# Performance work log

Hardware: AMD Instinct MI355X
Metric: run time of the kernel (lower is better)

## Reference

```python
import jax, jax.numpy as jnp
import numpy as np

N_G, N_U, E, C = 100000, 100000, 3200000, 2000000


def graph_conv(x, edges, W_rel, W_root, b):
    # PyG GraphConv (aggr='add'): out_i = (sum_{j->i} x_j) @ W_rel + x_i @ W_root + b
    src, dst = edges[0], edges[1]
    agg = jax.ops.segment_sum(x[src], dst, num_segments=x.shape[0])
    return agg @ W_rel + x @ W_root + b


def setup_inputs() -> dict:
    key = jax.random.key(0)
    ks = jax.random.split(key, 16)
    d = {
        'x_u': jax.random.normal(ks[0], (N_U, 4), jnp.float32),
        'x_g': jax.random.normal(ks[1], (N_G, 4), jnp.float32),
        'candidates': jax.random.randint(ks[2], (C, 2), 0, N_G + N_U, jnp.int64),
        'edges': jax.random.randint(ks[3], (2, E), 0, N_G, jnp.int64),
        # GraphConv(4,8)
        'W1_rel': jax.random.normal(ks[4], (4, 8), jnp.float32) * 0.5,
        'W1_root': jax.random.normal(ks[5], (4, 8), jnp.float32) * 0.5,
        'b1': jax.random.normal(ks[6], (8,), jnp.float32) * 0.1,
        # GraphConv(8,16)
        'W2_rel': jax.random.normal(ks[7], (8, 16), jnp.float32) * 0.35,
        'W2_root': jax.random.normal(ks[8], (8, 16), jnp.float32) * 0.35,
        'b2': jax.random.normal(ks[9], (16,), jnp.float32) * 0.1,
        # fc_unconnected: Linear(4,16) (Dropout is identity in eval)
        'W_un': jax.random.normal(ks[10], (4, 16), jnp.float32) * 0.5,
        'b_un': jax.random.normal(ks[11], (16,), jnp.float32) * 0.1,
        # fc: Linear(32,64) -> SELU -> Linear(64,1)
        'W_fc1': jax.random.normal(ks[12], (32, 64), jnp.float32) * 0.18,
        'b_fc1': jax.random.normal(ks[13], (64,), jnp.float32) * 0.1,
        'W_fc2': jax.random.normal(ks[14], (64, 1), jnp.float32) * 0.12,
        'b_fc2': jax.random.normal(ks[15], (1,), jnp.float32) * 0.1,
    }
    return d


def reference(x_u, x_g, candidates, edges,
              W1_rel, W1_root, b1, W2_rel, W2_root, b2,
              W_un, b_un, W_fc1, b_fc1, W_fc2, b_fc2):
    x_unconnected = x_u @ W_un + b_un                      # [N_u, 16]
    h = jax.nn.selu(graph_conv(x_g, edges, W1_rel, W1_root, b1))   # [N_g, 8]
    x_graph = jax.nn.selu(graph_conv(h, edges, W2_rel, W2_root, b2))  # [N_g, 16]
    x_stacked = jnp.concatenate([x_graph, x_unconnected], axis=0)  # [N_g+N_u, 16]
    ec = jnp.concatenate([x_stacked[candidates[:, 0]],
                          x_stacked[candidates[:, 1]]], axis=1)    # [C, 32]
    hidden = jax.nn.selu(ec @ W_fc1 + b_fc1)               # [C, 64]
    out = (hidden @ W_fc2 + b_fc2).squeeze(-1)             # [C]
    return out


if __name__ == '__main__':
    print(reference(**setup_inputs()).shape)
```

## Files before the change

kernel.cpp:

```cpp
#include <hip/hip_runtime.h>
#include <hip/hip_bf16.h>

#define NG 100000
#define NU 100000
#define NE 3200000
#define NC 2000000

#define BSZ 128
#define NBK 782
#define CAP 5120
#define B1CH 4096

typedef __attribute__((ext_vector_type(8))) short short8;
typedef __attribute__((ext_vector_type(4))) float floatx4;
typedef unsigned short ushortx8 __attribute__((ext_vector_type(8)));

__device__ __forceinline__ float selu_f(float x) {
    const float LAM = 1.0507009873554805f;
    const float ALA = 1.7580993408473766f;
    const float L2E = 1.44269504088896340736f;
    float e = __builtin_amdgcn_exp2f(fminf(x, 0.f) * L2E);
    return fmaf(LAM, fmaxf(x, 0.f), fmaf(ALA, e, -ALA));
}

__device__ __forceinline__ float bfbits2f(unsigned short u) {
    return __uint_as_float(((unsigned)u) << 16);
}

__device__ __forceinline__ unsigned short f2bfbits(float f) {
    union { __hip_bfloat16 h; unsigned short u; } cv;
    cv.h = __float2bfloat16(f);
    return cv.u;
}

__device__ __forceinline__ float ldf(const void* p, int i, int isbf) {
    return isbf ? bfbits2f(((const unsigned short*)p)[i]) : ((const float*)p)[i];
}

__global__ __launch_bounds__(256) void k_bin1(const void* __restrict__ edges,
        int* __restrict__ gcur, unsigned int* __restrict__ glist) {
    __shared__ unsigned int tmp[B1CH];
    __shared__ unsigned short tfid[B1CH];
    __shared__ int hist[NBK];
    __shared__ int gbase[NBK];
    __shared__ int ofs[NBK];
    __shared__ int se64;

    int tid = threadIdx.x;
    long long base = (long long)blockIdx.x * B1CH;
    int chunk = (int)(NE - base);
    if (chunk > B1CH) chunk = B1CH;

    if (tid < 64) {
        unsigned long long m3 =
            __ballot(((const unsigned int*)edges)[2 * tid + 1] == 0u);
        if (tid == 0) se64 = (__popcll(m3) >= 48) ? 1 : 0;
    }
    for (int b = tid; b < NBK; b += 256) hist[b] = 0;
    __syncthreads();
    int e64 = se64;

    for (int i = 0; i < B1CH / 512; ++i) {
        int idx = i * 512 + tid * 2;
        if (idx < chunk) {
            int s0, s1, d0, d1;
            if (e64) {
                const long long* el = (const long long*)edges;
                longlong2 sv = *(const longlong2*)(el + base + idx);
                longlong2 dv = *(const longlong2*)(el + NE + base + idx);
                s0 = (int)sv.x; s1 = (int)sv.y;
                d0 = (int)dv.x; d1 = (int)dv.y;
            } else {
                const int* ei = (const int*)edges;
                int2 sv = *(const int2*)(ei + base + idx);
                int2 dv = *(const int2*)(ei + NE + base + idx);
                s0 = sv.x; s1 = sv.y; d0 = dv.x; d1 = dv.y;
            }
            int f0 = d0 >> 7;
            tmp[idx] = ((unsigned)s0 << 7) | (unsigned)(d0 & 127);
            tfid[idx] = (unsigned short)f0;
            atomicAdd(&hist[f0], 1);
            if (idx + 1 < chunk) {
                int f1 = d1 >> 7;
                tmp[idx + 1] = ((unsigned)s1 << 7) | (unsigned)(d1 & 127);
                tfid[idx + 1] = (unsigned short)f1;
                atomicAdd(&hist[f1], 1);
            }
        }
    }
    __syncthreads();

    for (int b = tid; b < NBK; b += 256) {
        int c = hist[b];
        gbase[b] = (c > 0) ? atomicAdd(&gcur[b], c) : 0;
        ofs[b] = 0;
    }
    __syncthreads();

    for (int i = 0; i < B1CH / 256; ++i) {
        int idx = i * 256 + tid;
        if (idx < chunk) {
            int f = tfid[idx];
            int pos = atomicAdd(&ofs[f], 1);
            int p = gbase[f] + pos;
            if (p < CAP) glist[(long long)f * CAP + p] = tmp[idx];
        }
    }
}

__global__ __launch_bounds__(256) void k_sort(const int* __restrict__ gcur,
        unsigned int* __restrict__ glist,
        int* __restrict__ dstoff, int* __restrict__ ddeg,
        const unsigned int* __restrict__ xw, const unsigned int* __restrict__ cw,
        const unsigned int* __restrict__ ew, int* __restrict__ flags) {
    __shared__ unsigned int tmp[CAP];
    __shared__ int hist[BSZ];
    __shared__ int cur[BSZ];
    __shared__ int wtot;
    int b = blockIdx.x;
    int tid = threadIdx.x;

    if (b == 0 && tid < 64) {
        unsigned lo = xw[tid] & 0xffffu;
        unsigned e = (lo >> 7) & 0xff;
        unsigned long long m1 = __ballot(e >= 112 && e <= 134);
        unsigned long long m2 = __ballot(cw[2 * tid + 1] == 0u);
        unsigned long long m3 = __ballot(ew[2 * tid + 1] == 0u);
        if (tid == 0) {
            flags[0] = (__popcll(m1) >= 32) ? 1 : 0;
            flags[1] = (__popcll(m2) >= 48) ? 1 : 0;
            flags[2] = (__popcll(m3) >= 48) ? 1 : 0;
        }
    }

    int cnt = gcur[b];
    if (cnt > CAP) cnt = CAP;
    unsigned int* lp = glist + (long long)b * CAP;

    if (tid < BSZ) hist[tid] = 0;
    __syncthreads();
    for (int k = tid; k < cnt; k += 256) {
        unsigned u = lp[k];
        tmp[k] = u;
        atomicAdd(&hist[u & 127], 1);
    }
    __syncthreads();
    int h = (tid < BSZ) ? hist[tid] : 0;
    int s = h;
#pragma unroll
    for (int off = 1; off < 64; off <<= 1) {
        int v = __shfl_up(s, off, 64);
        if ((tid & 63) >= off) s += v;
    }
    if (tid == 63) wtot = s;
    __syncthreads();
    if (tid >= 64 && tid < BSZ) s += wtot;
    if (tid < BSZ) {
        int excl = s - h;
        cur[tid] = excl;
        int d = b * BSZ + tid;
        if (d < NG) {
            dstoff[d] = b * CAP + excl;
            ddeg[d] = h;
        }
    }
    __syncthreads();
    for (int k = tid; k < cnt; k += 256) {
        unsigned u = tmp[k];
        int pos = atomicAdd(&cur[u & 127], 1);
        lp[pos] = u >> 7;
    }
}

__global__ __launch_bounds__(256) void k_gather1(const int* __restrict__ dstoff,
        const int* __restrict__ ddeg, const unsigned int* __restrict__ glist,
        const void* __restrict__ xg,
        const void* __restrict__ W1r, const void* __restrict__ W1o,
        const void* __restrict__ b1, unsigned short* __restrict__ hbf,
        const int* __restrict__ flags) {
    int gid = blockIdx.x * 256 + threadIdx.x;
    int d = gid >> 4;
    if (d >= NG) return;
    int q = gid & 15;
    int isbf = flags[0];
    int start = dstoff[d];
    int deg = ddeg[d];
    float a0 = 0.f, a1 = 0.f, a2 = 0.f, a3 = 0.f;
    if (isbf) {
        const unsigned short* xp = (const unsigned short*)xg;
        int k = q;
        for (; k + 16 < deg; k += 32) {
            int s0 = glist[start + k];
            int s1 = glist[start + k + 16];
            ushort4 r0 = *(const ushort4*)(xp + s0 * 4);
            ushort4 r1 = *(const ushort4*)(xp + s1 * 4);
            a0 += bfbits2f(r0.x) + bfbits2f(r1.x);
            a1 += bfbits2f(r0.y) + bfbits2f(r1.y);
            a2 += bfbits2f(r0.z) + bfbits2f(r1.z);
            a3 += bfbits2f(r0.w) + bfbits2f(r1.w);
        }
        for (; k < deg; k += 16) {
            int s = glist[start + k];
            ushort4 r = *(const ushort4*)(xp + s * 4);
            a0 += bfbits2f(r.x); a1 += bfbits2f(r.y);
            a2 += bfbits2f(r.z); a3 += bfbits2f(r.w);
        }
    } else {
        const float* xp = (const float*)xg;
        int k = q;
        for (; k + 16 < deg; k += 32) {
            int s0 = glist[start + k];
            int s1 = glist[start + k + 16];
            float4 r0 = *(const float4*)(xp + s0 * 4);
            float4 r1 = *(const float4*)(xp + s1 * 4);
            a0 += r0.x + r1.x;
            a1 += r0.y + r1.y;
            a2 += r0.z + r1.z;
            a3 += r0.w + r1.w;
        }
        for (; k < deg; k += 16) {
            int s = glist[start + k];
            float4 r = *(const float4*)(xp + s * 4);
            a0 += r.x; a1 += r.y; a2 += r.z; a3 += r.w;
        }
    }
#pragma unroll
    for (int off = 1; off < 16; off <<= 1) {
        a0 += __shfl_xor(a0, off);
        a1 += __shfl_xor(a1, off);
        a2 += __shfl_xor(a2, off);
        a3 += __shfl_xor(a3, off);
    }
    if (q < 8) {
        float a[4] = {a0, a1, a2, a3};
        float v = ldf(b1, q, isbf);
#pragma unroll
        for (int c = 0; c < 4; ++c)
            v += a[c] * ldf(W1r, c * 8 + q, isbf)
               + ldf(xg, d * 4 + c, isbf) * ldf(W1o, c * 8 + q, isbf);
        hbf[d * 8 + q] = f2bfbits(selu_f(v));
    }
}

#define G2BLK ((16 * NG + 255) / 256)
#define UCBLK ((NU + 255) / 256)

__global__ __launch_bounds__(256) void k_gather2(const int* __restrict__ dstoff,
        const int* __restrict__ ddeg, const unsigned int* __restrict__ glist,
        const ushortx8* __restrict__ hbf,
        const void* __restrict__ W2r, const void* __restrict__ W2o,
        const void* __restrict__ b2, unsigned short* __restrict__ xs,
        const void* __restrict__ xu, const void* __restrict__ Wun,
        const void* __restrict__ bun, const int* __restrict__ flags) {
    int isbf = flags[0];
    if (blockIdx.x >= G2BLK) {
        int u = (blockIdx.x - G2BLK) * 256 + threadIdx.x;
        if (u >= NU) return;
        float x[4];
#pragma unroll
        for (int k = 0; k < 4; ++k) x[k] = ldf(xu, u * 4 + k, isbf);
        ushortx8 lo, hi;
#pragma unroll
        for (int j = 0; j < 16; ++j) {
            float v = ldf(bun, j, isbf);
#pragma unroll
            for (int k = 0; k < 4; ++k)
                v += x[k] * ldf(Wun, k * 16 + j, isbf);
            unsigned short bb = f2bfbits(v);
            if (j < 8) lo[j] = bb; else hi[j - 8] = bb;
        }
        ushortx8* xp = (ushortx8*)(xs + (NG + u) * 16);
        xp[0] = lo;
        xp[1] = hi;
        return;
    }
    int gid = blockIdx.x * 256 + threadIdx.x;
    int d = gid >> 4;
    if (d >= NG) return;
    int q = gid & 15;
    int start = dstoff[d];
    int deg = ddeg[d];
    float a[8] = {0.f, 0.f, 0.f, 0.f, 0.f, 0.f, 0.f, 0.f};
    int k = q;
    for (; k + 16 < deg; k += 32) {
        int s0 = glist[start + k];
        int s1 = glist[start + k + 16];
        ushortx8 r0 = hbf[s0];
        ushortx8 r1 = hbf[s1];
#pragma unroll
        for (int c = 0; c < 8; ++c)
            a[c] += bfbits2f((unsigned short)r0[c]) + bfbits2f((unsigned short)r1[c]);
    }
    for (; k < deg; k += 16) {
        int s = glist[start + k];
        ushortx8 r = hbf[s];
#pragma unroll
        for (int c = 0; c < 8; ++c) a[c] += bfbits2f((unsigned short)r[c]);
    }
#pragma unroll
    for (int off = 1; off < 16; off <<= 1) {
#pragma unroll
        for (int c = 0; c < 8; ++c) a[c] += __shfl_xor(a[c], off);
    }
    ushortx8 hr = hbf[d];
    float hv[8];
#pragma unroll
    for (int c = 0; c < 8; ++c) hv[c] = bfbits2f((unsigned short)hr[c]);
    float v = ldf(b2, q, isbf);
#pragma unroll
    for (int c = 0; c < 8; ++c)
        v += a[c] * ldf(W2r, c * 16 + q, isbf)
           + hv[c] * ldf(W2o, c * 16 + q, isbf);
    xs[d * 16 + q] = f2bfbits(selu_f(v));
}

__device__ __forceinline__ int ld_candrow(const void* cand, int c, int hp, int c64) {
    const int* ci = (const int*)cand;
    return c64 ? ci[(2 * c + hp) * 2] : ci[2 * c + hp];
}

__global__ __launch_bounds__(256, 5) void k_fc(const unsigned short* __restrict__ xs,
        const void* __restrict__ cand,
        const void* __restrict__ Wfc1, const void* __restrict__ bfc1,
        const void* __restrict__ Wfc2, const void* __restrict__ bfc2,
        void* __restrict__ out, const int* __restrict__ flags,
        int t0, int t1) {
    const float LAM = 1.0507009873554805f;
    const float ALA = 1.7580993408473766f;
    const float L2E = 1.44269504088896340736f;
    const float AR2 = 1.6732632423543772f * 1.44269504088896340736f;
    const float SCL = 1.0507009873554805f / 1.44269504088896340736f;
    int lane = threadIdx.x & 63;
    int wid = (blockIdx.x * blockDim.x + threadIdx.x) >> 6;
    int m = lane & 15;
    int half = lane >> 4;
    int isbf = flags[0], c64 = flags[1];

    short8 wfrag[4];
    floatx4 cbias[4];
    float w2s[4][4];
    float c_corr;
    if (isbf) {
        const unsigned short* W1p = (const unsigned short*)Wfc1;
#pragma unroll
        for (int t = 0; t < 4; ++t)
#pragma unroll
            for (int j = 0; j < 8; ++j)
                wfrag[t][j] = (short)f2bfbits(
                    bfbits2f(W1p[(half * 8 + j) * 64 + t * 16 + m]) * L2E);
        const unsigned short* b1p = (const unsigned short*)bfc1;
        const unsigned short* w2p = (const unsigned short*)Wfc2;
        float asum = 0.f;
#pragma unroll
        for (int t = 0; t < 4; ++t)
#pragma unroll
            for (int r = 0; r < 4; ++r) {
                int h = t * 16 + half * 4 + r;
                cbias[t][r] = bfbits2f(b1p[h]) * L2E;
                float w2 = bfbits2f(w2p[h]);
                w2s[t][r] = w2 * SCL;
                asum += w2 * ALA;
            }
        asum += __shfl_xor(asum, 16, 64);
        asum += __shfl_xor(asum, 32, 64);
        c_corr = bfbits2f(((const unsigned short*)bfc2)[0]) - asum;
    } else {
        const float* W1p = (const float*)Wfc1;
#pragma unroll
        for (int t = 0; t < 4; ++t)
#pragma unroll
            for (int j = 0; j < 8; ++j)
                wfrag[t][j] = (short)f2bfbits(
                    W1p[(half * 8 + j) * 64 + t * 16 + m] * L2E);
        const float* b1p = (const float*)bfc1;
        const float* w2p = (const float*)Wfc2;
        float asum = 0.f;
#pragma unroll
        for (int t = 0; t < 4; ++t)
#pragma unroll
            for (int r = 0; r < 4; ++r) {
                int h = t * 16 + half * 4 + r;
                cbias[t][r] = b1p[h] * L2E;
                float w2 = w2p[h];
                w2s[t][r] = w2 * SCL;
                asum += w2 * ALA;
            }
        asum += __shfl_xor(asum, 16, 64);
        asum += __shfl_xor(asum, 32, 64);
        c_corr = ((const float*)bfc2)[0] - asum;
    }

    int nW = (gridDim.x * blockDim.x) >> 6;
    if (t0 + wid >= t1) return;
    int tw = t0 + wid;

    int half1 = half & 1;
    int hp = half >> 1;
    int q1 = tw + nW, q2 = tw + 2 * nW, q3 = tw + 3 * nW, q4 = tw + 4 * nW;
    int r0i = ld_candrow(cand, tw * 16 + m, hp, c64);
    int r1i = ld_candrow(cand, ((q1 < t1) ? q1 : tw) * 16 + m, hp, c64);
    int r2i = ld_candrow(cand, ((q2 < t1) ? q2 : tw) * 16 + m, hp, c64);
    int r3i = ld_candrow(cand, ((q3 < t1) ? q3 : tw) * 16 + m, hp, c64);
    int r4i = ld_candrow(cand, ((q4 < t1) ? q4 : tw) * 16 + m, hp, c64);
    {
        short8 af0 = *(const short8*)(xs + r0i * 16 + half1 * 8);
        short8 af1 = *(const short8*)(xs + r1i * 16 + half1 * 8);
        short8 af2 = *(const short8*)(xs + r2i * 16 + half1 * 8);
        short8 af3 = *(const short8*)(xs + r3i * 16 + half1 * 8);

#pragma unroll 2
        for (int t = tw; t < t1; t += nW) {
            int tn5 = t + 5 * nW;
            int r5i = ld_candrow(cand, ((tn5 < t1) ? tn5 : t) * 16 + m, hp, c64);
            short8 af4 = *(const short8*)(xs + r4i * 16 + half1 * 8);

            float ps[4];
#pragma unroll
            for (int tt = 0; tt < 4; ++tt) {
                floatx4 ac = __builtin_amdgcn_mfma_f32_16x16x32_bf16(
                    wfrag[tt], af0, cbias[tt], 0, 0, 0);
                float s = 0.f;
#pragma unroll
                for (int r = 0; r < 4; ++r) {
                    float v = ac[r];
                    float mx = fmaxf(v, 0.f);
                    float e = __builtin_amdgcn_exp2f(fminf(v, 0.f));
                    s = fmaf(w2s[tt][r], fmaf(AR2, e, mx), s);
                }
                ps[tt] = s;
            }
            float part = (ps[0] + ps[1]) + (ps[2] + ps[3]);
            part += __shfl_xor(part, 16, 64);
            part += __shfl_xor(part, 32, 64);
            if (half == 0) {
                float o = part + c_corr;
                if (isbf) ((unsigned short*)out)[t * 16 + m] = f2bfbits(o);
                else ((float*)out)[t * 16 + m] = o;
            }
            af0 = af1;
            af1 = af2;
            af2 = af3;
            af3 = af4;
            r4i = r5i;
        }
    }
}

extern "C" void kernel_launch(void* const* d_in, const int* in_sizes, int n_in,
                              void* d_out, int out_size, void* d_ws, size_t ws_size,
                              hipStream_t stream) {
    const void* x_u = d_in[0];
    const void* x_g = d_in[1];
    const void* cand = d_in[2];
    const void* edges = d_in[3];
    const void* W1r = d_in[4];
    const void* W1o = d_in[5];
    const void* b1 = d_in[6];
    const void* W2r = d_in[7];
    const void* W2o = d_in[8];
    const void* b2 = d_in[9];
    const void* Wun = d_in[10];
    const void* bun = d_in[11];
    const void* Wfc1 = d_in[12];
    const void* bfc1 = d_in[13];
    const void* Wfc2 = d_in[14];
    const void* bfc2 = d_in[15];

    char* ws = (char*)d_ws;
    int* flags = (int*)ws;
    int* gcur = (int*)(ws + 64);
    unsigned int* glist = (unsigned int*)(ws + 4160);
    size_t glist_bytes = (size_t)NBK * CAP * 4;
    char* p = ws + 4160 + glist_bytes;
    int* dstoff = (int*)p;
    int* ddeg = (int*)(p + 400000);
    unsigned short* hbf = (unsigned short*)(p + 800000);
    unsigned short* xs = (unsigned short*)(p + 2400000);

    hipMemsetAsync(gcur, 0, 3200, stream);

    k_bin1<<<(NE + B1CH - 1) / B1CH, 256, 0, stream>>>(edges, gcur, glist);
    k_sort<<<NBK, 256, 0, stream>>>(gcur, glist, dstoff, ddeg,
                                    (const unsigned int*)x_u,
                                    (const unsigned int*)cand,
                                    (const unsigned int*)edges, flags);
    k_gather1<<<(16 * NG + 255) / 256, 256, 0, stream>>>(dstoff, ddeg, glist, x_g,
                                                         W1r, W1o, b1, hbf, flags);
    k_gather2<<<G2BLK + UCBLK, 256, 0, stream>>>(dstoff, ddeg, glist,
                                                 (const ushortx8*)hbf,
                                                 W2r, W2o, b2, xs,
                                                 x_u, Wun, bun, flags);
    const int nTiles = NC / 16;
    const int tMid = nTiles / 2;
    k_fc<<<1280, 256, 0, stream>>>(xs, cand, Wfc1, bfc1, Wfc2, bfc2, d_out, flags,
                                   0, tMid);
    k_fc<<<1280, 256, 0, stream>>>(xs, cand, Wfc1, bfc1, Wfc2, bfc2, d_out, flags,
                                   tMid, nTiles);
}
```

Baseline: 261.9 us.

## Replace bucketed binning+sort CSR build with count/scan/atomic scatter

```diff
diff --git a/kernel.cpp b/kernel.cpp
--- a/kernel.cpp
+++ b/kernel.cpp
@@ -9,7 +9,6 @@
 #define BSZ 128
 #define NBK 782
 #define CAP 5120
-#define B1CH 4096
 
 typedef __attribute__((ext_vector_type(8))) short short8;
 typedef __attribute__((ext_vector_type(4))) float floatx4;
@@ -37,86 +36,38 @@
     return isbf ? bfbits2f(((const unsigned short*)p)[i]) : ((const float*)p)[i];
 }
 
-__global__ __launch_bounds__(256) void k_bin1(const void* __restrict__ edges,
-        int* __restrict__ gcur, unsigned int* __restrict__ glist) {
-    __shared__ unsigned int tmp[B1CH];
-    __shared__ unsigned short tfid[B1CH];
-    __shared__ int hist[NBK];
-    __shared__ int gbase[NBK];
-    __shared__ int ofs[NBK];
+__global__ __launch_bounds__(256) void k_count(const void* __restrict__ edges,
+        int* __restrict__ ddeg) {
     __shared__ int se64;
-
     int tid = threadIdx.x;
-    long long base = (long long)blockIdx.x * B1CH;
-    int chunk = (int)(NE - base);
-    if (chunk > B1CH) chunk = B1CH;
-
     if (tid < 64) {
         unsigned long long m3 =
             __ballot(((const unsigned int*)edges)[2 * tid + 1] == 0u);
         if (tid == 0) se64 = (__popcll(m3) >= 48) ? 1 : 0;
     }
-    for (int b = tid; b < NBK; b += 256) hist[b] = 0;
     __syncthreads();
     int e64 = se64;
-
-    for (int i = 0; i < B1CH / 512; ++i) {
-        int idx = i * 512 + tid * 2;
-        if (idx < chunk) {
-            int s0, s1, d0, d1;
-            if (e64) {
-                const long long* el = (const long long*)edges;
-                longlong2 sv = *(const longlong2*)(el + base + idx);
-                longlong2 dv = *(const longlong2*)(el + NE + base + idx);
-                s0 = (int)sv.x; s1 = (int)sv.y;
-                d0 = (int)dv.x; d1 = (int)dv.y;
-            } else {
-                const int* ei = (const int*)edges;
-                int2 sv = *(const int2*)(ei + base + idx);
-                int2 dv = *(const int2*)(ei + NE + base + idx);
-                s0 = sv.x; s1 = sv.y; d0 = dv.x; d1 = dv.y;
-            }
-            int f0 = d0 >> 7;
-            tmp[idx] = ((unsigned)s0 << 7) | (unsigned)(d0 & 127);
-            tfid[idx] = (unsigned short)f0;
-            atomicAdd(&hist[f0], 1);
-            if (idx + 1 < chunk) {
-                int f1 = d1 >> 7;
-                tmp[idx + 1] = ((unsigned)s1 << 7) | (unsigned)(d1 & 127);
-                tfid[idx + 1] = (unsigned short)f1;
-                atomicAdd(&hist[f1], 1);
-            }
-        }
-    }
-    __syncthreads();
-
-    for (int b = tid; b < NBK; b += 256) {
-        int c = hist[b];
-        gbase[b] = (c > 0) ? atomicAdd(&gcur[b], c) : 0;
-        ofs[b] = 0;
-    }
-    __syncthreads();
-
-    for (int i = 0; i < B1CH / 256; ++i) {
-        int idx = i * 256 + tid;
-        if (idx < chunk) {
-            int f = tfid[idx];
-            int pos = atomicAdd(&ofs[f], 1);
-            int p = gbase[f] + pos;
-            if (p < CAP) glist[(long long)f * CAP + p] = tmp[idx];
-        }
-    }
-}
-
-__global__ __launch_bounds__(256) void k_sort(const int* __restrict__ gcur,
-        unsigned int* __restrict__ glist,
-        int* __restrict__ dstoff, int* __restrict__ ddeg,
+    long long i = ((long long)blockIdx.x * 256 + tid) * 2;
+    if (i >= NE) return;
+    int d0, d1;
+    if (e64) {
+        const long long* el = (const long long*)edges;
+        longlong2 dv = *(const longlong2*)(el + NE + i);
+        d0 = (int)dv.x; d1 = (int)dv.y;
+    } else {
+        const int* ei = (const int*)edges;
+        int2 dv = *(const int2*)(ei + NE + i);
+        d0 = dv.x; d1 = dv.y;
+    }
+    atomicAdd(&ddeg[d0], 1);
+    atomicAdd(&ddeg[d1], 1);
+}
+
+__global__ __launch_bounds__(128) void k_scan(int* __restrict__ ddeg,
+        int* __restrict__ dstoff, int* __restrict__ cur,
         const unsigned int* __restrict__ xw, const unsigned int* __restrict__ cw,
         const unsigned int* __restrict__ ew, int* __restrict__ flags) {
-    __shared__ unsigned int tmp[CAP];
-    __shared__ int hist[BSZ];
-    __shared__ int cur[BSZ];
-    __shared__ int wtot;
+    __shared__ int w0sum;
     int b = blockIdx.x;
     int tid = threadIdx.x;
 
@@ -133,43 +84,59 @@
         }
     }
 
-    int cnt = gcur[b];
-    if (cnt > CAP) cnt = CAP;
-    unsigned int* lp = glist + (long long)b * CAP;
-
-    if (tid < BSZ) hist[tid] = 0;
-    __syncthreads();
-    for (int k = tid; k < cnt; k += 256) {
-        unsigned u = lp[k];
-        tmp[k] = u;
-        atomicAdd(&hist[u & 127], 1);
-    }
-    __syncthreads();
-    int h = (tid < BSZ) ? hist[tid] : 0;
-    int s = h;
+    int d = b * BSZ + tid;
+    int deg = (d < NG) ? ddeg[d] : 0;
+    int s = deg;
 #pragma unroll
     for (int off = 1; off < 64; off <<= 1) {
         int v = __shfl_up(s, off, 64);
         if ((tid & 63) >= off) s += v;
     }
-    if (tid == 63) wtot = s;
+    if (tid == 63) w0sum = s;
     __syncthreads();
-    if (tid >= 64 && tid < BSZ) s += wtot;
-    if (tid < BSZ) {
-        int excl = s - h;
-        cur[tid] = excl;
-        int d = b * BSZ + tid;
-        if (d < NG) {
-            dstoff[d] = b * CAP + excl;
-            ddeg[d] = h;
-        }
+    if (tid >= 64) s += w0sum;
+    if (d < NG) {
+        int excl = s - deg;
+        int e2 = (excl < CAP) ? excl : CAP;
+        int room = CAP - e2;
+        int dcap = (deg < room) ? deg : room;
+        int abs0 = b * CAP + e2;
+        dstoff[d] = abs0;
+        ddeg[d] = dcap;
+        cur[d] = abs0;
+    }
+}
+
+__global__ __launch_bounds__(256) void k_scatter(const void* __restrict__ edges,
+        int* __restrict__ cur, unsigned int* __restrict__ glist) {
+    __shared__ int se64;
+    int tid = threadIdx.x;
+    if (tid < 64) {
+        unsigned long long m3 =
+            __ballot(((const unsigned int*)edges)[2 * tid + 1] == 0u);
+        if (tid == 0) se64 = (__popcll(m3) >= 48) ? 1 : 0;
     }
     __syncthreads();
-    for (int k = tid; k < cnt; k += 256) {
-        unsigned u = tmp[k];
-        int pos = atomicAdd(&cur[u & 127], 1);
-        lp[pos] = u >> 7;
-    }
+    int e64 = se64;
+    long long i = ((long long)blockIdx.x * 256 + tid) * 2;
+    if (i >= NE) return;
+    int s0, s1, d0, d1;
+    if (e64) {
+        const long long* el = (const long long*)edges;
+        longlong2 sv = *(const longlong2*)(el + i);
+        longlong2 dv = *(const longlong2*)(el + NE + i);
+        s0 = (int)sv.x; s1 = (int)sv.y;
+        d0 = (int)dv.x; d1 = (int)dv.y;
+    } else {
+        const int* ei = (const int*)edges;
+        int2 sv = *(const int2*)(ei + i);
+        int2 dv = *(const int2*)(ei + NE + i);
+        s0 = sv.x; s1 = sv.y; d0 = dv.x; d1 = dv.y;
+    }
+    int p0 = atomicAdd(&cur[d0], 1);
+    int p1 = atomicAdd(&cur[d1], 1);
+    if (p0 < ((d0 >> 7) + 1) * CAP) glist[p0] = (unsigned)s0;
+    if (p1 < ((d1 >> 7) + 1) * CAP) glist[p1] = (unsigned)s1;
 }
 
 __global__ __launch_bounds__(256) void k_gather1(const int* __restrict__ dstoff,
@@ -468,22 +435,24 @@
 
     char* ws = (char*)d_ws;
     int* flags = (int*)ws;
-    int* gcur = (int*)(ws + 64);
-    unsigned int* glist = (unsigned int*)(ws + 4160);
+    int* ddeg = (int*)(ws + 64);
+    int* dstoff = (int*)(ws + 400064);
+    int* cur = (int*)(ws + 800064);
+    unsigned int* glist = (unsigned int*)(ws + 1200064);
     size_t glist_bytes = (size_t)NBK * CAP * 4;
-    char* p = ws + 4160 + glist_bytes;
-    int* dstoff = (int*)p;
-    int* ddeg = (int*)(p + 400000);
-    unsigned short* hbf = (unsigned short*)(p + 800000);
-    unsigned short* xs = (unsigned short*)(p + 2400000);
-
-    hipMemsetAsync(gcur, 0, 3200, stream);
-
-    k_bin1<<<(NE + B1CH - 1) / B1CH, 256, 0, stream>>>(edges, gcur, glist);
-    k_sort<<<NBK, 256, 0, stream>>>(gcur, glist, dstoff, ddeg,
+    char* p = ws + 1200064 + glist_bytes;
+    unsigned short* hbf = (unsigned short*)p;
+    unsigned short* xs = (unsigned short*)(p + 1600000);
+
+    hipMemsetAsync(ddeg, 0, 400000, stream);
+
+    const int EPBLK = (NE / 2 + 255) / 256;
+    k_count<<<EPBLK, 256, 0, stream>>>(edges, ddeg);
+    k_scan<<<NBK, 128, 0, stream>>>(ddeg, dstoff, cur,
                                     (const unsigned int*)x_u,
                                     (const unsigned int*)cand,
                                     (const unsigned int*)edges, flags);
+    k_scatter<<<EPBLK, 256, 0, stream>>>(edges, cur, glist);
     k_gather1<<<(16 * NG + 255) / 256, 256, 0, stream>>>(dstoff, ddeg, glist, x_g,
                                                          W1r, W1o, b1, hbf, flags);
     k_gather2<<<G2BLK + UCBLK, 256, 0, stream>>>(dstoff, ddeg, glist,
```

New measurement: 617.1 us. 2.36x slower.
